# Kernel optimization log

Measured on AMD Instinct MI355X. Metric: run time of the kernel, lower is better.

The kernel has to match this reference:

```python
import jax, jax.numpy as jnp
import numpy as np

N_TAGS = 256
SOS, EOS, PAD = 0, 1, 2
NEG = -1000000.0
B, T = 256, 512


def _init_transitions(key):
    t = jax.random.uniform(key, (N_TAGS, N_TAGS), jnp.float32, -0.1, 0.1)
    t = t.at[:, SOS].set(NEG)
    t = t.at[EOS, :].set(NEG)
    t = t.at[PAD, :].set(NEG)
    t = t.at[:, PAD].set(NEG)
    t = t.at[PAD, EOS].set(0.0)
    t = t.at[PAD, PAD].set(0.0)
    return t


def setup_inputs() -> dict:
    key = jax.random.key(0)
    k_em, k_tr = jax.random.split(key)
    emissions = jax.random.normal(k_em, (B, T, N_TAGS), jnp.float32)
    mask = jnp.ones((B, T), jnp.float32)
    transitions = _init_transitions(k_tr)
    return {"emissions": emissions, "mask": mask, "transitions": transitions}


def reference(emissions, mask, transitions):
    # Viterbi decode: max-plus DP over seq_len, then vectorized backtrace.
    # emissions: [B, T, n], mask: [B, T] float, transitions: [n, n]
    alphas0 = transitions[SOS][None, :] + emissions[:, 0]  # [B, n]
    em_rest = jnp.moveaxis(emissions[:, 1:], 1, 0)          # [T-1, B, n]
    m_rest = mask[:, 1:].T                                  # [T-1, B]

    def step(alphas, inp):
        em_t, m_t = inp
        # scores[b, prev, cur] = alphas[b, prev] + transitions[prev, cur] + em_t[b, cur]
        scores = alphas[:, :, None] + transitions[None, :, :] + em_t[:, None, :]
        max_scores = jnp.max(scores, axis=1)                 # [B, n]
        bpt = jnp.argmax(scores, axis=1).astype(jnp.int32)   # [B, n]
        new_alphas = m_t[:, None] * max_scores + (1.0 - m_t[:, None]) * alphas
        return new_alphas, bpt

    alphas, backptrs = jax.lax.scan(step, alphas0, (em_rest, m_rest))  # backptrs: [T-1, B, n]

    end_scores = alphas + transitions[:, EOS][None, :]       # [B, n]
    best_scores = jnp.max(end_scores, axis=1)                # [B]
    final_tags = jnp.argmax(end_scores, axis=1).astype(jnp.int32)  # [B]

    def back_step(tag, bpt):
        # tag: best tag at position t+1 ; bpt[b, tag] -> best tag at position t
        new_tag = jnp.take_along_axis(bpt, tag[:, None], axis=1)[:, 0]
        return new_tag, new_tag

    _, prev_tags = jax.lax.scan(back_step, final_tags, backptrs, reverse=True)
    # prev_tags: [T-1, B] in forward time order (tags for positions 0..T-2)
    paths = jnp.concatenate([prev_tags.T, final_tags[:, None]], axis=1)  # [B, T]
    return best_scores, paths
```

## Files before the change

### kernel.cpp

```cpp
#include <hip/hip_runtime.h>

#define NTAGS  256
#define TLEN   512
#define BATCH  256
#define QS     68
#define NEGINF (-3.0e38f)

__global__ __launch_bounds__(1024, 4)
void viterbi_dp(const float* __restrict__ emis,
                const float* __restrict__ mask,
                const float* __restrict__ trans,
                float* __restrict__ out)
{
    __shared__ __align__(16) float aSh[2][4 * QS];
    __shared__ unsigned char bptL[(TLEN - 1) * NTAGS];
    __shared__ float endS[NTAGS];

    const int tid   = threadIdx.x;
    const int w     = tid >> 6;
    const int lane  = tid & 63;
    const int c     = (w << 4) | (lane & 15);
    const int h     = lane >> 4;
    const int pbase = h << 6;
    const int b     = blockIdx.x;

    float treg[64];
#pragma unroll
    for (int p = 0; p < 64; ++p) {
        treg[p] = trans[(pbase + p) * NTAGS + c];
        asm volatile("" : "+v"(treg[p]));
    }

    const float* eb = emis + (size_t)b * TLEN * NTAGS;
    const float* mb = mask + (size_t)b * TLEN;

    float aOld = trans[c] + eb[c];
    if (h == 0) aSh[0][QS * (c >> 6) + (c & 63)] = aOld;
    __syncthreads();

    float emCur = eb[NTAGS + c];
    float mCur  = mb[1];

    int cur = 0;
    for (int t = 1; t < TLEN; ++t) {
        float emNext = 0.0f, mNext = 1.0f;
        if (t + 1 < TLEN) {
            emNext = eb[(t + 1) * NTAGS + c];
            mNext  = mb[t + 1];
        }

        const float4* a4 = (const float4*)(&aSh[cur][h * QS]);
        float gb = NEGINF;
        int   ga = 0;
#pragma unroll
        for (int q = 0; q < 16; ++q) {
            const float4 al = a4[q];
            float s;
            s = (al.x + treg[4 * q + 0]) + emCur; if (s > gb) { gb = s; ga = 4 * q + 0; }
            s = (al.y + treg[4 * q + 1]) + emCur; if (s > gb) { gb = s; ga = 4 * q + 1; }
            s = (al.z + treg[4 * q + 2]) + emCur; if (s > gb) { gb = s; ga = 4 * q + 2; }
            s = (al.w + treg[4 * q + 3]) + emCur; if (s > gb) { gb = s; ga = 4 * q + 3; }
        }
        ga += pbase;

#pragma unroll
        for (int m = 16; m <= 32; m <<= 1) {
            const float pvv = __shfl_xor(gb, m, 64);
            const int   paa = __shfl_xor(ga, m, 64);
            const bool take = (pvv > gb) || ((pvv == gb) && (paa < ga));
            gb = take ? pvv : gb;
            ga = take ? paa : ga;
        }

        const float aNew = mCur * gb + (1.0f - mCur) * aOld;
        if (h == 0)      aSh[cur ^ 1][QS * (c >> 6) + (c & 63)] = aNew;
        else if (h == 1) bptL[(t - 1) * NTAGS + c] = (unsigned char)ga;

        aOld  = aNew;
        emCur = emNext;
        mCur  = mNext;
        cur  ^= 1;
        __syncthreads();
    }

    if (h == 0) endS[c] = aOld + trans[c * NTAGS + 1];
    __syncthreads();

    if (tid == 0) {
        float best = endS[0]; int arg = 0;
        for (int i = 1; i < NTAGS; ++i) {
            float v = endS[i];
            if (v > best) { best = v; arg = i; }
        }
        out[b] = best;

        float* pout = out + BATCH + (size_t)b * TLEN;
        int tag = arg;
        pout[TLEN - 1] = (float)tag;
        for (int t = TLEN - 2; t >= 0; --t) {
            tag = bptL[t * NTAGS + tag];
            pout[t] = (float)tag;
        }
    }
}

extern "C" void kernel_launch(void* const* d_in, const int* in_sizes, int n_in,
                              void* d_out, int out_size, void* d_ws, size_t ws_size,
                              hipStream_t stream) {
    (void)d_ws; (void)ws_size; (void)in_sizes; (void)n_in; (void)out_size;
    const float* emis  = (const float*)d_in[0];
    const float* mask  = (const float*)d_in[1];
    const float* trans = (const float*)d_in[2];
    float* out = (float*)d_out;

    viterbi_dp<<<dim3(BATCH), dim3(1024), 0, stream>>>(emis, mask, trans, out);
}
```

Baseline: 1.186 ms.

## Give each thread two output tags over 32 prev tags to halve alpha LDS reads

Work is redistributed so each lane handles two current tags (cA, cB) over a 32-element slice of previous tags, with 8 slices per wave instead of 4 slices of 64. Each alpha float4 read from shared memory is reused for two output columns, which halves LDS read traffic per score. Each column's max is split into independent lo/hi chains to shorten the dependent compare chain. The cost is one extra butterfly shuffle stage with twice the shuffles per stage, and a new padded shared layout (BLK=36) that changes the bank pattern.

Result: slower. 1.530 ms (+29.0%).

```diff
diff --git a/kernel.cpp b/kernel.cpp
--- a/kernel.cpp
+++ b/kernel.cpp
@@ -3,7 +3,7 @@
 #define NTAGS  256
 #define TLEN   512
 #define BATCH  256
-#define QS     68
+#define BLK    36
 #define NEGINF (-3.0e38f)
 
 __global__ __launch_bounds__(1024, 4)
@@ -12,78 +12,113 @@
                 const float* __restrict__ trans,
                 float* __restrict__ out)
 {
-    __shared__ __align__(16) float aSh[2][4 * QS];
+    __shared__ __align__(16) float aSh[2][8 * BLK];
     __shared__ unsigned char bptL[(TLEN - 1) * NTAGS];
     __shared__ float endS[NTAGS];
 
-    const int tid   = threadIdx.x;
-    const int w     = tid >> 6;
-    const int lane  = tid & 63;
-    const int c     = (w << 4) | (lane & 15);
-    const int h     = lane >> 4;
-    const int pbase = h << 6;
-    const int b     = blockIdx.x;
+    const int tid  = threadIdx.x;
+    const int w    = tid >> 6;
+    const int lane = tid & 63;
+    const int g    = lane >> 3;
+    const int j    = lane & 7;
+    const int cA   = (w << 4) + j;
+    const int cB   = cA + 8;
+    const int pb   = g << 5;
+    const int b    = blockIdx.x;
 
-    float treg[64];
+    float trA[32], trB[32];
 #pragma unroll
-    for (int p = 0; p < 64; ++p) {
-        treg[p] = trans[(pbase + p) * NTAGS + c];
-        asm volatile("" : "+v"(treg[p]));
+    for (int p = 0; p < 32; ++p) {
+        trA[p] = trans[(pb + p) * NTAGS + cA];
+        trB[p] = trans[(pb + p) * NTAGS + cB];
     }
 
     const float* eb = emis + (size_t)b * TLEN * NTAGS;
     const float* mb = mask + (size_t)b * TLEN;
 
-    float aOld = trans[c] + eb[c];
-    if (h == 0) aSh[0][QS * (c >> 6) + (c & 63)] = aOld;
+    float aOldA = trans[cA] + eb[cA];
+    float aOldB = trans[cB] + eb[cB];
+    if (g == 0) {
+        aSh[0][(cA >> 5) * BLK + (cA & 31)] = aOldA;
+        aSh[0][(cB >> 5) * BLK + (cB & 31)] = aOldB;
+    }
     __syncthreads();
 
-    float emCur = eb[NTAGS + c];
-    float mCur  = mb[1];
+    float emA = eb[NTAGS + cA], emB = eb[NTAGS + cB];
+    float mCur = mb[1];
 
     int cur = 0;
     for (int t = 1; t < TLEN; ++t) {
-        float emNext = 0.0f, mNext = 1.0f;
+        float emA2 = 0.0f, emB2 = 0.0f, mNext = 1.0f;
         if (t + 1 < TLEN) {
-            emNext = eb[(t + 1) * NTAGS + c];
-            mNext  = mb[t + 1];
+            emA2  = eb[(t + 1) * NTAGS + cA];
+            emB2  = eb[(t + 1) * NTAGS + cB];
+            mNext = mb[t + 1];
         }
 
-        const float4* a4 = (const float4*)(&aSh[cur][h * QS]);
-        float gb = NEGINF;
-        int   ga = 0;
+        const float4* aBlk = (const float4*)(&aSh[cur][g * BLK]);
+
+        float mAlo = NEGINF, mAhi = NEGINF, mBlo = NEGINF, mBhi = NEGINF;
+        int   gAlo = 0,      gAhi = 16,     gBlo = 0,      gBhi = 16;
 #pragma unroll
-        for (int q = 0; q < 16; ++q) {
-            const float4 al = a4[q];
+        for (int q = 0; q < 4; ++q) {
+            const float4 lo = aBlk[q];
+            const float4 hi = aBlk[q + 4];
             float s;
-            s = (al.x + treg[4 * q + 0]) + emCur; if (s > gb) { gb = s; ga = 4 * q + 0; }
-            s = (al.y + treg[4 * q + 1]) + emCur; if (s > gb) { gb = s; ga = 4 * q + 1; }
-            s = (al.z + treg[4 * q + 2]) + emCur; if (s > gb) { gb = s; ga = 4 * q + 2; }
-            s = (al.w + treg[4 * q + 3]) + emCur; if (s > gb) { gb = s; ga = 4 * q + 3; }
+            s = (lo.x + trA[4*q+0])  + emA; if (s > mAlo) { mAlo = s; gAlo = 4*q+0; }
+            s = (lo.y + trA[4*q+1])  + emA; if (s > mAlo) { mAlo = s; gAlo = 4*q+1; }
+            s = (lo.z + trA[4*q+2])  + emA; if (s > mAlo) { mAlo = s; gAlo = 4*q+2; }
+            s = (lo.w + trA[4*q+3])  + emA; if (s > mAlo) { mAlo = s; gAlo = 4*q+3; }
+            s = (hi.x + trA[16+4*q+0]) + emA; if (s > mAhi) { mAhi = s; gAhi = 16+4*q+0; }
+            s = (hi.y + trA[16+4*q+1]) + emA; if (s > mAhi) { mAhi = s; gAhi = 16+4*q+1; }
+            s = (hi.z + trA[16+4*q+2]) + emA; if (s > mAhi) { mAhi = s; gAhi = 16+4*q+2; }
+            s = (hi.w + trA[16+4*q+3]) + emA; if (s > mAhi) { mAhi = s; gAhi = 16+4*q+3; }
+            s = (lo.x + trB[4*q+0])  + emB; if (s > mBlo) { mBlo = s; gBlo = 4*q+0; }
+            s = (lo.y + trB[4*q+1])  + emB; if (s > mBlo) { mBlo = s; gBlo = 4*q+1; }
+            s = (lo.z + trB[4*q+2])  + emB; if (s > mBlo) { mBlo = s; gBlo = 4*q+2; }
+            s = (lo.w + trB[4*q+3])  + emB; if (s > mBlo) { mBlo = s; gBlo = 4*q+3; }
+            s = (hi.x + trB[16+4*q+0]) + emB; if (s > mBhi) { mBhi = s; gBhi = 16+4*q+0; }
+            s = (hi.y + trB[16+4*q+1]) + emB; if (s > mBhi) { mBhi = s; gBhi = 16+4*q+1; }
+            s = (hi.z + trB[16+4*q+2]) + emB; if (s > mBhi) { mBhi = s; gBhi = 16+4*q+2; }
+            s = (hi.w + trB[16+4*q+3]) + emB; if (s > mBhi) { mBhi = s; gBhi = 16+4*q+3; }
         }
-        ga += pbase;
+        float vA = (mAhi > mAlo) ? mAhi : mAlo;
+        int   iA = ((mAhi > mAlo) ? gAhi : gAlo) + pb;
+        float vB = (mBhi > mBlo) ? mBhi : mBlo;
+        int   iB = ((mBhi > mBlo) ? gBhi : gBlo) + pb;
 
 #pragma unroll
-        for (int m = 16; m <= 32; m <<= 1) {
-            const float pvv = __shfl_xor(gb, m, 64);
-            const int   paa = __shfl_xor(ga, m, 64);
-            const bool take = (pvv > gb) || ((pvv == gb) && (paa < ga));
-            gb = take ? pvv : gb;
-            ga = take ? paa : ga;
+        for (int m = 8; m <= 32; m <<= 1) {
+            const float pvA = __shfl_xor(vA, m, 64);
+            const int   piA = __shfl_xor(iA, m, 64);
+            const float pvB = __shfl_xor(vB, m, 64);
+            const int   piB = __shfl_xor(iB, m, 64);
+            bool tk = (pvA > vA) || ((pvA == vA) && (piA < iA));
+            vA = tk ? pvA : vA;  iA = tk ? piA : iA;
+            tk = (pvB > vB) || ((pvB == vB) && (piB < iB));
+            vB = tk ? pvB : vB;  iB = tk ? piB : iB;
         }
 
-        const float aNew = mCur * gb + (1.0f - mCur) * aOld;
-        if (h == 0)      aSh[cur ^ 1][QS * (c >> 6) + (c & 63)] = aNew;
-        else if (h == 1) bptL[(t - 1) * NTAGS + c] = (unsigned char)ga;
+        const float aNewA = mCur * vA + (1.0f - mCur) * aOldA;
+        const float aNewB = mCur * vB + (1.0f - mCur) * aOldB;
+        if (g == 0) {
+            aSh[cur ^ 1][(cA >> 5) * BLK + (cA & 31)] = aNewA;
+            aSh[cur ^ 1][(cB >> 5) * BLK + (cB & 31)] = aNewB;
+        } else if (g == 1) {
+            bptL[(t - 1) * NTAGS + cA] = (unsigned char)iA;
+            bptL[(t - 1) * NTAGS + cB] = (unsigned char)iB;
+        }
 
-        aOld  = aNew;
-        emCur = emNext;
-        mCur  = mNext;
-        cur  ^= 1;
+        aOldA = aNewA;  aOldB = aNewB;
+        emA = emA2;  emB = emB2;  mCur = mNext;
+        cur ^= 1;
         __syncthreads();
     }
 
-    if (h == 0) endS[c] = aOld + trans[c * NTAGS + 1];
+    if (g == 0) {
+        endS[cA] = aOldA + trans[cA * NTAGS + 1];
+        endS[cB] = aOldB + trans[cB * NTAGS + 1];
+    }
     __syncthreads();
 
     if (tid == 0) {
```
